# Kernel tuning notes

Hardware: AMD Instinct MI355X
Metric: run time of the kernel (lower is better)

## Reference

```python
import jax, jax.numpy as jnp
import numpy as np

N_NODES = 50000
N_EDGES = 25000
NNZ = 800000
IN_DIM = 256
OUT_DIM = 256


def setup_inputs() -> dict:
    key = jax.random.key(0)
    k1, k2, k3, k4, k5 = jax.random.split(key, 5)
    X = jax.random.normal(k1, (N_NODES, IN_DIM), dtype=jnp.float32)
    node_idx = jax.random.randint(k2, (NNZ,), 0, N_NODES, dtype=jnp.int64)
    edge_idx = jax.random.randint(k3, (NNZ,), 0, N_EDGES, dtype=jnp.int64)
    # Xavier-uniform-ish weight, zero bias (matches reset_parameters)
    limit = float(np.sqrt(6.0 / (IN_DIM + OUT_DIM)))
    W = jax.random.uniform(k4, (IN_DIM, OUT_DIM), dtype=jnp.float32, minval=-limit, maxval=limit)
    b = jnp.zeros((OUT_DIM,), dtype=jnp.float32)
    return {"X": X, "node_idx": node_idx, "edge_idx": edge_idx, "W": W, "b": b}


def reference(X, node_idx, edge_idx, W, b):
    # Y = X @ W + b  -- dense GEMM
    Y = X @ W + b  # [N, out_dim]

    ones = jnp.ones(node_idx.shape[0], dtype=Y.dtype)
    # D_v = rowsum(H)^-0.5 (inf -> 0); D_e = colsum(H)^-1 (inf -> 0)
    deg_v = jax.ops.segment_sum(ones, node_idx, num_segments=N_NODES)
    deg_e = jax.ops.segment_sum(ones, edge_idx, num_segments=N_EDGES)
    d_v = jnp.where(deg_v > 0, deg_v ** -0.5, 0.0)  # [N]
    d_e = jnp.where(deg_e > 0, 1.0 / deg_e, 0.0)    # [E]

    # step1 = H^T @ (D_v X): gather scaled node rows, scatter-add into edges
    Z = d_v[:, None] * Y                                   # [N, out_dim]
    step1 = jax.ops.segment_sum(Z[node_idx], edge_idx, num_segments=N_EDGES)  # [E, out_dim]
    # step2 = D_e @ step1
    step2 = d_e[:, None] * step1                           # [E, out_dim]
    # step3 = H @ step2: gather edge rows, scatter-add into nodes
    step3 = jax.ops.segment_sum(step2[edge_idx], node_idx, num_segments=N_NODES)  # [N, out_dim]
    # final = D_v @ step3
    return d_v[:, None] * step3
```

## Files before the change

kernel.cpp:

```cpp
#include <hip/hip_runtime.h>

#define N_NODES 50000
#define N_EDGES 25000
#define NNZ     800000
#define DIM     256

#define CAP_E 88
#define CAP_V 56

#define NBE 98
#define NBV 196
#define CE_COARSE 8800
#define CV_COARSE 4500
#define NNZ_PB 2048
#define P1_BLOCKS 391

#define B_A1   0
#define B_CE   0
#define B_CV   3449600
#define B_CSRE 12800000
#define B_CSRV 17200000
#define B_WT   22800000
#define B_CURV 22931072
#define B_CURE 23131072
#define B_CCUR 23331072
#define B_DV   23332248

typedef __attribute__((ext_vector_type(8))) short s8v;
typedef __attribute__((ext_vector_type(4))) float f4v;

__device__ __forceinline__ unsigned short f2bf(float f) {
    unsigned u = __float_as_uint(f);
    u = (u + 0x7FFFu + ((u >> 16) & 1u)) >> 16;
    return (unsigned short)u;
}
__device__ __forceinline__ float bf2f(unsigned short h) {
    return __uint_as_float(((unsigned)h) << 16);
}

__global__ __launch_bounds__(256) void k_prep(
        const float* __restrict__ W,
        const int* __restrict__ node_idx, const int* __restrict__ edge_idx,
        unsigned short* __restrict__ WTb,
        unsigned* __restrict__ ccurE, unsigned* __restrict__ ccurV,
        unsigned* __restrict__ coarseE, unsigned* __restrict__ coarseV) {
    if (blockIdx.x < 32) {
        int t = blockIdx.x * 256 + threadIdx.x;
        int n = t >> 5;
        int k0 = (t & 31) * 8;
        unsigned short o[8];
#pragma unroll
        for (int j = 0; j < 8; ++j) o[j] = f2bf(W[(size_t)(k0 + j) * DIM + n]);
        *(s8v*)(WTb + (size_t)n * DIM + k0) = *(const s8v*)o;
        return;
    }

    __shared__ unsigned histE[NBE], histV[NBV], baseE[NBE], baseV[NBV];
    __shared__ unsigned offE[NBE], offV[NBV];
    __shared__ unsigned nEs, nVs;
    __shared__ unsigned bufE[NNZ_PB], dstE[NNZ_PB];
    __shared__ unsigned bufV[NNZ_PB], dstV[NNZ_PB];
    const int tid = threadIdx.x;
    const int pb  = blockIdx.x - 32;
    const int base = pb * NNZ_PB;

    if (tid < NBE) histE[tid] = 0;
    if (tid < NBV) histV[tid] = 0;
    __syncthreads();

    int idx0 = base + tid * 4;
    int idx1 = base + 1024 + tid * 4;
    bool ok0 = idx0 < NNZ, ok1 = idx1 < NNZ;
    int4 v0 = ok0 ? *(const int4*)(node_idx + idx0) : (int4){0,0,0,0};
    int4 e0 = ok0 ? *(const int4*)(edge_idx + idx0) : (int4){0,0,0,0};
    int4 v1 = ok1 ? *(const int4*)(node_idx + idx1) : (int4){0,0,0,0};
    int4 e1 = ok1 ? *(const int4*)(edge_idx + idx1) : (int4){0,0,0,0};
    int vv[8] = {v0.x, v0.y, v0.z, v0.w, v1.x, v1.y, v1.z, v1.w};
    int ee[8] = {e0.x, e0.y, e0.z, e0.w, e1.x, e1.y, e1.z, e1.w};

    unsigned short locE[8], locV[8];
#pragma unroll
    for (int j = 0; j < 8; ++j) {
        bool ok = (j < 4) ? ok0 : ok1;
        if (ok) {
            locE[j] = (unsigned short)atomicAdd(&histE[ee[j] >> 8], 1u);
            locV[j] = (unsigned short)atomicAdd(&histV[vv[j] >> 8], 1u);
        }
    }
    __syncthreads();
    if (tid < NBE) baseE[tid] = atomicAdd(&ccurE[tid], histE[tid]);
    if (tid < NBV) baseV[tid] = atomicAdd(&ccurV[tid], histV[tid]);
    if (tid == 0) { unsigned r = 0; for (int b = 0; b < NBE; ++b) { offE[b] = r; r += histE[b]; } nEs = r; }
    if (tid == 1) { unsigned r = 0; for (int b = 0; b < NBV; ++b) { offV[b] = r; r += histV[b]; } nVs = r; }
    __syncthreads();

#pragma unroll
    for (int j = 0; j < 8; ++j) {
        bool ok = (j < 4) ? ok0 : ok1;
        if (ok) {
            unsigned e = (unsigned)ee[j], v = (unsigned)vv[j];
            unsigned be = e >> 8, bv = v >> 8;
            unsigned se = offE[be] + locE[j];
            unsigned pe = baseE[be] + locE[j];
            bufE[se] = ((e & 255u) << 16) | v;
            dstE[se] = (pe < CE_COARSE) ? (be * CE_COARSE + pe) : 0xFFFFFFFFu;
            unsigned sv = offV[bv] + locV[j];
            unsigned pv = baseV[bv] + locV[j];
            bufV[sv] = ((v & 255u) << 16) | e;
            dstV[sv] = (pv < CV_COARSE) ? (bv * CV_COARSE + pv) : 0xFFFFFFFFu;
        }
    }
    __syncthreads();

    unsigned nE = nEs, nV = nVs;
    for (unsigned i = tid; i < nE; i += 256) {
        unsigned d = dstE[i];
        if (d != 0xFFFFFFFFu) coarseE[d] = bufE[i];
    }
    for (unsigned i = tid; i < nV; i += 256) {
        unsigned d = dstV[i];
        if (d != 0xFFFFFFFFu) coarseV[d] = bufV[i];
    }
}

__global__ __launch_bounds__(1024) void k_fine(
        const unsigned* __restrict__ coarseE, const unsigned* __restrict__ coarseV,
        const unsigned* __restrict__ ccurE, const unsigned* __restrict__ ccurV,
        unsigned short* __restrict__ csrE, unsigned short* __restrict__ csrV,
        unsigned* __restrict__ cur_e, unsigned* __restrict__ cur_v,
        float* __restrict__ dv) {
    __shared__ unsigned cnt[256];
    __shared__ unsigned short slots[256 * CAP_E];
    const int tid = threadIdx.x;
    if (tid < 256) cnt[tid] = 0;
    __syncthreads();

    if (blockIdx.x < NBE) {
        int b = blockIdx.x;
        unsigned n = ccurE[b]; n = n < CE_COARSE ? n : CE_COARSE;
        const unsigned* src = coarseE + (size_t)b * CE_COARSE;
        for (unsigned i = tid; i < n; i += 1024) {
            unsigned p = src[i];
            unsigned f = p >> 16, v = p & 0xFFFFu;
            unsigned pos = atomicAdd(&cnt[f], 1u);
            if (pos < CAP_E) slots[f * CAP_E + pos] = (unsigned short)v;
        }
        __syncthreads();
        if (tid < 256) {
            int e = b * 256 + tid;
            if (e < N_EDGES) cur_e[e] = cnt[tid];
        }
        int rows = N_EDGES - b * 256; rows = rows < 256 ? rows : 256;
        unsigned words = (unsigned)rows * (CAP_E / 2);
        unsigned* dst = (unsigned*)(csrE + (size_t)b * 256 * CAP_E);
        const unsigned* s = (const unsigned*)slots;
        for (unsigned i = tid; i < words; i += 1024) dst[i] = s[i];
    } else {
        int b = blockIdx.x - NBE;
        unsigned n = ccurV[b]; n = n < CV_COARSE ? n : CV_COARSE;
        const unsigned* src = coarseV + (size_t)b * CV_COARSE;
        for (unsigned i = tid; i < n; i += 1024) {
            unsigned p = src[i];
            unsigned f = p >> 16, e = p & 0xFFFFu;
            unsigned pos = atomicAdd(&cnt[f], 1u);
            if (pos < CAP_V) slots[f * CAP_V + pos] = (unsigned short)e;
        }
        __syncthreads();
        if (tid < 256) {
            int v = b * 256 + tid;
            if (v < N_NODES) {
                unsigned c = cnt[tid];
                cur_v[v] = c;
                dv[v] = c ? __frsqrt_rn((float)c) : 0.0f;
            }
        }
        int rows = N_NODES - b * 256; rows = rows < 256 ? rows : 256;
        unsigned words = (unsigned)rows * (CAP_V / 2);
        unsigned* dst = (unsigned*)(csrV + (size_t)b * 256 * CAP_V);
        const unsigned* s = (const unsigned*)slots;
        for (unsigned i = tid; i < words; i += 1024) dst[i] = s[i];
    }
}

__global__ __launch_bounds__(256) void k_gemm_y(
        const float* __restrict__ X,
        const unsigned short* __restrict__ WT,
        const float* __restrict__ bias,
        unsigned short* __restrict__ Yb) {
    __shared__ unsigned short As[64][264];
    const int tid  = threadIdx.x;
    const int wv   = tid >> 6;
    const int lane = tid & 63;
    const int quad = lane >> 4;
    const int l16  = lane & 15;
    const int r0   = blockIdx.x * 64;
    const int nb   = wv * 64;

#pragma unroll
    for (int it = 0; it < 16; ++it) {
        int i   = tid + it * 256;
        int row = i >> 6;
        int c4  = i & 63;
        int src = r0 + row;
        src = (src < N_NODES) ? src : (N_NODES - 1);
        float4 p = *(const float4*)(X + (size_t)src * DIM + c4 * 4);
        unsigned short o[4] = {f2bf(p.x), f2bf(p.y), f2bf(p.z), f2bf(p.w)};
        *(ushort4*)(&As[row][c4 * 4]) = *(const ushort4*)o;
    }
    __syncthreads();

    f4v acc[4][4];
#pragma unroll
    for (int mt = 0; mt < 4; ++mt)
#pragma unroll
        for (int nt = 0; nt < 4; ++nt) acc[mt][nt] = (f4v){0.f, 0.f, 0.f, 0.f};

    for (int k0 = 0; k0 < DIM; k0 += 32) {
        s8v a[4], b[4];
#pragma unroll
        for (int nt = 0; nt < 4; ++nt) {
            int n = nb + nt * 16 + l16;
            b[nt] = *(const s8v*)(WT + (size_t)n * DIM + k0 + quad * 8);
        }
#pragma unroll
        for (int mt = 0; mt < 4; ++mt)
            a[mt] = *(const s8v*)(&As[mt * 16 + l16][k0 + quad * 8]);
#pragma unroll
        for (int mt = 0; mt < 4; ++mt)
#pragma unroll
            for (int nt = 0; nt < 4; ++nt)
                acc[mt][nt] = __builtin_amdgcn_mfma_f32_16x16x32_bf16(
                    a[mt], b[nt], acc[mt][nt], 0, 0, 0);
    }

    float bv[4];
#pragma unroll
    for (int nt = 0; nt < 4; ++nt) bv[nt] = bias[nb + nt * 16 + l16];

#pragma unroll
    for (int mt = 0; mt < 4; ++mt) {
#pragma unroll
        for (int reg = 0; reg < 4; ++reg) {
            int row = r0 + mt * 16 + quad * 4 + reg;
            if (row < N_NODES) {
#pragma unroll
                for (int nt = 0; nt < 4; ++nt) {
                    Yb[(size_t)row * DIM + nb + nt * 16 + l16] =
                        f2bf(acc[mt][nt][reg] + bv[nt]);
                }
            }
        }
    }
}

__global__ __launch_bounds__(256) void k_gather_edges(
        const unsigned short* __restrict__ Yb,
        const unsigned short* __restrict__ csrE,
        const unsigned* __restrict__ cur_e,
        const float* __restrict__ dv,
        unsigned short* __restrict__ S2) {
    int w = (blockIdx.x * 256 + threadIdx.x) >> 6;
    int lane = threadIdx.x & 63;
    if (w >= N_EDGES) return;
    unsigned deg = cur_e[w];
    unsigned cnt = deg < CAP_E ? deg : CAP_E;
    float sc = deg ? 1.0f / (float)deg : 0.0f;
    const unsigned short* lst = csrE + (size_t)w * CAP_E;
    unsigned idp = (lane < CAP_E / 2) ? ((const unsigned*)lst)[lane] : 0u;
    const unsigned short* xb = Yb + (size_t)lane * 4;

    float ax = 0.f, ay = 0.f, az = 0.f, aw = 0.f;

#define EFETCH(J, X0, X1, X2, X3, S0, S1, S2_, S3)                         \
    {                                                                      \
        unsigned p0 = __shfl(idp, (int)((J) >> 1));                        \
        unsigned p1 = __shfl(idp, (int)((J) >> 1) + 1);                    \
        unsigned v0 = p0 & 0xFFFFu, v1 = p0 >> 16;                         \
        unsigned v2 = p1 & 0xFFFFu, v3 = p1 >> 16;                         \
        S0 = dv[v0]; S1 = dv[v1]; S2_ = dv[v2]; S3 = dv[v3];               \
        X0 = *(const ushort4*)(xb + ((size_t)v0 << 8));                    \
        X1 = *(const ushort4*)(xb + ((size_t)v1 << 8));                    \
        X2 = *(const ushort4*)(xb + ((size_t)v2 << 8));                    \
        X3 = *(const ushort4*)(xb + ((size_t)v3 << 8));                    \
    }
#define ECONS(X0, X1, X2, X3, S0, S1, S2_, S3)                             \
    {                                                                      \
        ax = fmaf(S0, bf2f(X0.x), ax); ay = fmaf(S0, bf2f(X0.y), ay);      \
        az = fmaf(S0, bf2f(X0.z), az); aw = fmaf(S0, bf2f(X0.w), aw);      \
        ax = fmaf(S1, bf2f(X1.x), ax); ay = fmaf(S1, bf2f(X1.y), ay);      \
        az = fmaf(S1, bf2f(X1.z), az); aw = fmaf(S1, bf2f(X1.w), aw);      \
        ax = fmaf(S2_, bf2f(X2.x), ax); ay = fmaf(S2_, bf2f(X2.y), ay);    \
        az = fmaf(S2_, bf2f(X2.z), az); aw = fmaf(S2_, bf2f(X2.w), aw);    \
        ax = fmaf(S3, bf2f(X3.x), ax); ay = fmaf(S3, bf2f(X3.y), ay);      \
        az = fmaf(S3, bf2f(X3.z), az); aw = fmaf(S3, bf2f(X3.w), aw);      \
    }

    unsigned quads = cnt >> 2;
    unsigned j = 0;
    if (quads) {
        ushort4 a0, a1, a2, a3, b0, b1, b2, b3;
        float r0, r1, r2, r3, t0, t1, t2, t3;
        EFETCH(0u, a0, a1, a2, a3, r0, r1, r2, r3);
        unsigned q = 1;
        for (; q + 1 < quads; q += 2) {
            EFETCH(4u * q,      b0, b1, b2, b3, t0, t1, t2, t3);
            ECONS(a0, a1, a2, a3, r0, r1, r2, r3);
            EFETCH(4u * q + 4u, a0, a1, a2, a3, r0, r1, r2, r3);
            ECONS(b0, b1, b2, b3, t0, t1, t2, t3);
        }
        if (q < quads) {
            EFETCH(4u * q, b0, b1, b2, b3, t0, t1, t2, t3);
            ECONS(a0, a1, a2, a3, r0, r1, r2, r3);
            ECONS(b0, b1, b2, b3, t0, t1, t2, t3);
        } else {
            ECONS(a0, a1, a2, a3, r0, r1, r2, r3);
        }
        j = quads << 2;
    }
    for (; j < cnt; ++j) {
        unsigned p = __shfl(idp, (int)(j >> 1));
        unsigned v = (j & 1) ? (p >> 16) : (p & 0xFFFFu);
        float s = dv[v];
        ushort4 x = *(const ushort4*)(xb + ((size_t)v << 8));
        ax = fmaf(s, bf2f(x.x), ax); ay = fmaf(s, bf2f(x.y), ay);
        az = fmaf(s, bf2f(x.z), az); aw = fmaf(s, bf2f(x.w), aw);
    }
#undef EFETCH
#undef ECONS

    ushort4 o = {f2bf(sc * ax), f2bf(sc * ay), f2bf(sc * az), f2bf(sc * aw)};
    *(ushort4*)(S2 + (size_t)w * DIM + lane * 4) = o;
}

__global__ __launch_bounds__(256) void k_gather_nodes(
        const unsigned short* __restrict__ S2,
        const unsigned short* __restrict__ csrV,
        const unsigned* __restrict__ cur_v,
        const float* __restrict__ dv,
        float* __restrict__ out) {
    int w = (blockIdx.x * 256 + threadIdx.x) >> 6;
    int lane = threadIdx.x & 63;
    if (w >= N_NODES) return;
    unsigned cnt = cur_v[w]; cnt = cnt < CAP_V ? cnt : CAP_V;
    const unsigned short* lst = csrV + (size_t)w * CAP_V;
    unsigned idp = (lane < CAP_V / 2) ? ((const unsigned*)lst)[lane] : 0u;
    const unsigned short* sb = S2 + (size_t)lane * 4;

    float ax = 0.f, ay = 0.f, az = 0.f, aw = 0.f;

#define NFETCH(J, X0, X1, X2, X3)                                          \
    {                                                                      \
        unsigned p0 = __shfl(idp, (int)((J) >> 1));                        \
        unsigned p1 = __shfl(idp, (int)((J) >> 1) + 1);                    \
        unsigned e0 = p0 & 0xFFFFu, e1 = p0 >> 16;                         \
        unsigned e2 = p1 & 0xFFFFu, e3 = p1 >> 16;                         \
        X0 = *(const ushort4*)(sb + ((size_t)e0 << 8));                    \
        X1 = *(const ushort4*)(sb + ((size_t)e1 << 8));                    \
        X2 = *(const ushort4*)(sb + ((size_t)e2 << 8));                    \
        X3 = *(const ushort4*)(sb + ((size_t)e3 << 8));                    \
    }
#define NCONS(X0, X1, X2, X3)                                              \
    {                                                                      \
        ax += (bf2f(X0.x) + bf2f(X1.x)) + (bf2f(X2.x) + bf2f(X3.x));       \
        ay += (bf2f(X0.y) + bf2f(X1.y)) + (bf2f(X2.y) + bf2f(X3.y));       \
        az += (bf2f(X0.z) + bf2f(X1.z)) + (bf2f(X2.z) + bf2f(X3.z));       \
        aw += (bf2f(X0.w) + bf2f(X1.w)) + (bf2f(X2.w) + bf2f(X3.w));       \
    }

    unsigned quads = cnt >> 2;
    unsigned j = 0;
    if (quads) {
        ushort4 a0, a1, a2, a3, b0, b1, b2, b3;
        NFETCH(0u, a0, a1, a2, a3);
        unsigned q = 1;
        for (; q + 1 < quads; q += 2) {
            NFETCH(4u * q,      b0, b1, b2, b3);
            NCONS(a0, a1, a2, a3);
            NFETCH(4u * q + 4u, a0, a1, a2, a3);
            NCONS(b0, b1, b2, b3);
        }
        if (q < quads) {
            NFETCH(4u * q, b0, b1, b2, b3);
            NCONS(a0, a1, a2, a3);
            NCONS(b0, b1, b2, b3);
        } else {
            NCONS(a0, a1, a2, a3);
        }
        j = quads << 2;
    }
    for (; j < cnt; ++j) {
        unsigned p = __shfl(idp, (int)(j >> 1));
        unsigned e = (j & 1) ? (p >> 16) : (p & 0xFFFFu);
        ushort4 x = *(const ushort4*)(sb + ((size_t)e << 8));
        ax += bf2f(x.x); ay += bf2f(x.y); az += bf2f(x.z); aw += bf2f(x.w);
    }
#undef NFETCH
#undef NCONS

    float s = dv[w];
    float4 o = {s * ax, s * ay, s * az, s * aw};
    *(float4*)(out + (size_t)w * DIM + lane * 4) = o;
}

extern "C" void kernel_launch(void* const* d_in, const int* in_sizes, int n_in,
                              void* d_out, int out_size, void* d_ws, size_t ws_size,
                              hipStream_t stream) {
    (void)in_sizes; (void)n_in; (void)out_size; (void)ws_size;
    const float* X        = (const float*)d_in[0];
    const int*   node_idx = (const int*)d_in[1];
    const int*   edge_idx = (const int*)d_in[2];
    const float* W        = (const float*)d_in[3];
    const float* bias     = (const float*)d_in[4];
    float* out = (float*)d_out;
    char*  ws  = (char*)d_ws;

    unsigned short* S2      = (unsigned short*)(ws + B_A1);
    unsigned*       coarseE = (unsigned*)(ws + B_CE);
    unsigned*       coarseV = (unsigned*)(ws + B_CV);
    unsigned short* csrE    = (unsigned short*)(ws + B_CSRE);
    unsigned short* csrV    = (unsigned short*)(ws + B_CSRV);
    unsigned short* WTb     = (unsigned short*)(ws + B_WT);
    unsigned*       cur_v   = (unsigned*)(ws + B_CURV);
    unsigned*       cur_e   = (unsigned*)(ws + B_CURE);
    unsigned*       ccurE   = (unsigned*)(ws + B_CCUR);
    unsigned*       ccurV   = ccurE + NBE;
    float*          dv      = (float*)(ws + B_DV);

    unsigned short* Yb = (unsigned short*)d_out;

    (void)hipMemsetAsync(ccurE, 0, (NBE + NBV) * sizeof(unsigned), stream);

    k_prep<<<32 + P1_BLOCKS, 256, 0, stream>>>(W, node_idx, edge_idx,
                                               WTb, ccurE, ccurV, coarseE, coarseV);
    k_fine<<<NBE + NBV, 1024, 0, stream>>>(coarseE, coarseV, ccurE, ccurV,
                                           csrE, csrV, cur_e, cur_v, dv);
    k_gemm_y<<<(N_NODES + 63) / 64, 256, 0, stream>>>(X, WTb, bias, Yb);
    k_gather_edges<<<(N_EDGES * 64 + 255) / 256, 256, 0, stream>>>(
        Yb, csrE, cur_e, dv, S2);
    k_gather_nodes<<<(N_NODES * 64 + 255) / 256, 256, 0, stream>>>(
        S2, csrV, cur_v, dv, out);
}
```

Before: 252.4 us.

## Merge GEMM and fine CSR bucketing into one launch, parallelize prefix scans

The dense X@W GEMM and the fine-grained CSR construction now run as one 1024-thread kernel. The first blocks each compute four 64-row GEMM tiles, staging K in two halves to fit shared memory, and the remaining blocks do the per-bucket fine sort. This removes one launch and lets the independent GEMM and CSR work overlap on the GPU. In the prep kernel the serial single-thread prefix sums over the bucket histograms become a parallel Hillis-Steele scan, and the CSR slot copy-out uses 16-byte stores. The trade-offs are extra barriers in the GEMM halves and larger 1024-thread GEMM blocks, which may lower occupancy.

```diff
diff --git a/kernel.cpp b/kernel.cpp
--- a/kernel.cpp
+++ b/kernel.cpp
@@ -14,6 +14,7 @@
 #define CV_COARSE 4500
 #define NNZ_PB 2048
 #define P1_BLOCKS 391
+#define GY_BLOCKS 196
 
 #define B_A1   0
 #define B_CE   0
@@ -57,6 +58,7 @@
 
     __shared__ unsigned histE[NBE], histV[NBV], baseE[NBE], baseV[NBV];
     __shared__ unsigned offE[NBE], offV[NBV];
+    __shared__ unsigned scanE[256], scanV[256];
     __shared__ unsigned nEs, nVs;
     __shared__ unsigned bufE[NNZ_PB], dstE[NNZ_PB];
     __shared__ unsigned bufV[NNZ_PB], dstV[NNZ_PB];
@@ -90,8 +92,20 @@
     __syncthreads();
     if (tid < NBE) baseE[tid] = atomicAdd(&ccurE[tid], histE[tid]);
     if (tid < NBV) baseV[tid] = atomicAdd(&ccurV[tid], histV[tid]);
-    if (tid == 0) { unsigned r = 0; for (int b = 0; b < NBE; ++b) { offE[b] = r; r += histE[b]; } nEs = r; }
-    if (tid == 1) { unsigned r = 0; for (int b = 0; b < NBV; ++b) { offV[b] = r; r += histV[b]; } nVs = r; }
+    scanE[tid] = (tid < NBE) ? histE[tid] : 0u;
+    scanV[tid] = (tid < NBV) ? histV[tid] : 0u;
+    __syncthreads();
+    for (int off = 1; off < 256; off <<= 1) {
+        unsigned tE = (tid >= off) ? scanE[tid - off] : 0u;
+        unsigned tV = (tid >= off) ? scanV[tid - off] : 0u;
+        __syncthreads();
+        scanE[tid] += tE;
+        scanV[tid] += tV;
+        __syncthreads();
+    }
+    if (tid < NBE) offE[tid] = scanE[tid] - histE[tid];
+    if (tid < NBV) offV[tid] = scanV[tid] - histV[tid];
+    if (tid == 0) { nEs = scanE[255]; nVs = scanV[255]; }
     __syncthreads();
 
 #pragma unroll
@@ -123,20 +137,100 @@
     }
 }
 
-__global__ __launch_bounds__(1024) void k_fine(
+__global__ __launch_bounds__(1024) void k_mid(
+        const float* __restrict__ X,
+        const unsigned short* __restrict__ WT,
+        const float* __restrict__ bias,
+        unsigned short* __restrict__ Yb,
         const unsigned* __restrict__ coarseE, const unsigned* __restrict__ coarseV,
         const unsigned* __restrict__ ccurE, const unsigned* __restrict__ ccurV,
         unsigned short* __restrict__ csrE, unsigned short* __restrict__ csrV,
         unsigned* __restrict__ cur_e, unsigned* __restrict__ cur_v,
         float* __restrict__ dv) {
-    __shared__ unsigned cnt[256];
-    __shared__ unsigned short slots[256 * CAP_E];
+    __shared__ __align__(16) char smem[69632];
     const int tid = threadIdx.x;
+
+    if (blockIdx.x < GY_BLOCKS) {
+        const int sub  = tid >> 8;
+        const int stid = tid & 255;
+        const int lane = stid & 63;
+        const int wv   = stid >> 6;
+        const int quad = lane >> 4;
+        const int l16  = lane & 15;
+        const int r0   = (blockIdx.x * 4 + sub) * 64;
+        const int nb   = wv * 64;
+        unsigned short (*As)[136] =
+            (unsigned short (*)[136])(smem + sub * 17408);
+
+        f4v acc[4][4];
+#pragma unroll
+        for (int mt = 0; mt < 4; ++mt)
+#pragma unroll
+            for (int nt = 0; nt < 4; ++nt) acc[mt][nt] = (f4v){0.f, 0.f, 0.f, 0.f};
+
+        for (int h = 0; h < 2; ++h) {
+            __syncthreads();
+#pragma unroll
+            for (int it = 0; it < 8; ++it) {
+                int i   = stid + it * 256;
+                int row = i >> 5;
+                int c4  = i & 31;
+                int src = r0 + row;
+                src = (src < N_NODES) ? src : (N_NODES - 1);
+                float4 p = *(const float4*)(X + (size_t)src * DIM + h * 128 + c4 * 4);
+                unsigned short o[4] = {f2bf(p.x), f2bf(p.y), f2bf(p.z), f2bf(p.w)};
+                *(ushort4*)(&As[row][c4 * 4]) = *(const ushort4*)o;
+            }
+            __syncthreads();
+
+            for (int k0l = 0; k0l < 128; k0l += 32) {
+                s8v a[4], b[4];
+#pragma unroll
+                for (int nt = 0; nt < 4; ++nt) {
+                    int n = nb + nt * 16 + l16;
+                    b[nt] = *(const s8v*)(WT + (size_t)n * DIM + h * 128 + k0l + quad * 8);
+                }
+#pragma unroll
+                for (int mt = 0; mt < 4; ++mt)
+                    a[mt] = *(const s8v*)(&As[mt * 16 + l16][k0l + quad * 8]);
+#pragma unroll
+                for (int mt = 0; mt < 4; ++mt)
+#pragma unroll
+                    for (int nt = 0; nt < 4; ++nt)
+                        acc[mt][nt] = __builtin_amdgcn_mfma_f32_16x16x32_bf16(
+                            a[mt], b[nt], acc[mt][nt], 0, 0, 0);
+            }
+        }
+
+        float bv[4];
+#pragma unroll
+        for (int nt = 0; nt < 4; ++nt) bv[nt] = bias[nb + nt * 16 + l16];
+
+#pragma unroll
+        for (int mt = 0; mt < 4; ++mt) {
+#pragma unroll
+            for (int reg = 0; reg < 4; ++reg) {
+                int row = r0 + mt * 16 + quad * 4 + reg;
+                if (row < N_NODES) {
+#pragma unroll
+                    for (int nt = 0; nt < 4; ++nt) {
+                        Yb[(size_t)row * DIM + nb + nt * 16 + l16] =
+                            f2bf(acc[mt][nt][reg] + bv[nt]);
+                    }
+                }
+            }
+        }
+        return;
+    }
+
+    unsigned*       cnt   = (unsigned*)smem;
+    unsigned short* slots = (unsigned short*)(smem + 1024);
+    const int fb = blockIdx.x - GY_BLOCKS;
     if (tid < 256) cnt[tid] = 0;
     __syncthreads();
 
-    if (blockIdx.x < NBE) {
-        int b = blockIdx.x;
+    if (fb < NBE) {
+        int b = fb;
         unsigned n = ccurE[b]; n = n < CE_COARSE ? n : CE_COARSE;
         const unsigned* src = coarseE + (size_t)b * CE_COARSE;
         for (unsigned i = tid; i < n; i += 1024) {
@@ -151,12 +245,12 @@
             if (e < N_EDGES) cur_e[e] = cnt[tid];
         }
         int rows = N_EDGES - b * 256; rows = rows < 256 ? rows : 256;
-        unsigned words = (unsigned)rows * (CAP_E / 2);
-        unsigned* dst = (unsigned*)(csrE + (size_t)b * 256 * CAP_E);
-        const unsigned* s = (const unsigned*)slots;
-        for (unsigned i = tid; i < words; i += 1024) dst[i] = s[i];
+        unsigned q4 = (unsigned)rows * (CAP_E / 2) / 4;
+        uint4* dst = (uint4*)(csrE + (size_t)b * 256 * CAP_E);
+        const uint4* s = (const uint4*)slots;
+        for (unsigned i = tid; i < q4; i += 1024) dst[i] = s[i];
     } else {
-        int b = blockIdx.x - NBE;
+        int b = fb - NBE;
         unsigned n = ccurV[b]; n = n < CV_COARSE ? n : CV_COARSE;
         const unsigned* src = coarseV + (size_t)b * CV_COARSE;
         for (unsigned i = tid; i < n; i += 1024) {
@@ -175,81 +269,10 @@
             }
         }
         int rows = N_NODES - b * 256; rows = rows < 256 ? rows : 256;
-        unsigned words = (unsigned)rows * (CAP_V / 2);
-        unsigned* dst = (unsigned*)(csrV + (size_t)b * 256 * CAP_V);
-        const unsigned* s = (const unsigned*)slots;
-        for (unsigned i = tid; i < words; i += 1024) dst[i] = s[i];
-    }
-}
-
-__global__ __launch_bounds__(256) void k_gemm_y(
-        const float* __restrict__ X,
-        const unsigned short* __restrict__ WT,
-        const float* __restrict__ bias,
-        unsigned short* __restrict__ Yb) {
-    __shared__ unsigned short As[64][264];
-    const int tid  = threadIdx.x;
-    const int wv   = tid >> 6;
-    const int lane = tid & 63;
-    const int quad = lane >> 4;
-    const int l16  = lane & 15;
-    const int r0   = blockIdx.x * 64;
-    const int nb   = wv * 64;
-
-#pragma unroll
-    for (int it = 0; it < 16; ++it) {
-        int i   = tid + it * 256;
-        int row = i >> 6;
-        int c4  = i & 63;
-        int src = r0 + row;
-        src = (src < N_NODES) ? src : (N_NODES - 1);
-        float4 p = *(const float4*)(X + (size_t)src * DIM + c4 * 4);
-        unsigned short o[4] = {f2bf(p.x), f2bf(p.y), f2bf(p.z), f2bf(p.w)};
-        *(ushort4*)(&As[row][c4 * 4]) = *(const ushort4*)o;
-    }
-    __syncthreads();
-
-    f4v acc[4][4];
-#pragma unroll
-    for (int mt = 0; mt < 4; ++mt)
-#pragma unroll
-        for (int nt = 0; nt < 4; ++nt) acc[mt][nt] = (f4v){0.f, 0.f, 0.f, 0.f};
-
-    for (int k0 = 0; k0 < DIM; k0 += 32) {
-        s8v a[4], b[4];
-#pragma unroll
-        for (int nt = 0; nt < 4; ++nt) {
-            int n = nb + nt * 16 + l16;
-            b[nt] = *(const s8v*)(WT + (size_t)n * DIM + k0 + quad * 8);
-        }
-#pragma unroll
-        for (int mt = 0; mt < 4; ++mt)
-            a[mt] = *(const s8v*)(&As[mt * 16 + l16][k0 + quad * 8]);
-#pragma unroll
-        for (int mt = 0; mt < 4; ++mt)
-#pragma unroll
-            for (int nt = 0; nt < 4; ++nt)
-                acc[mt][nt] = __builtin_amdgcn_mfma_f32_16x16x32_bf16(
-                    a[mt], b[nt], acc[mt][nt], 0, 0, 0);
-    }
-
-    float bv[4];
-#pragma unroll
-    for (int nt = 0; nt < 4; ++nt) bv[nt] = bias[nb + nt * 16 + l16];
-
-#pragma unroll
-    for (int mt = 0; mt < 4; ++mt) {
-#pragma unroll
-        for (int reg = 0; reg < 4; ++reg) {
-            int row = r0 + mt * 16 + quad * 4 + reg;
-            if (row < N_NODES) {
-#pragma unroll
-                for (int nt = 0; nt < 4; ++nt) {
-                    Yb[(size_t)row * DIM + nb + nt * 16 + l16] =
-                        f2bf(acc[mt][nt][reg] + bv[nt]);
-                }
-            }
-        }
+        unsigned q4 = (unsigned)rows * (CAP_V / 2) / 4;
+        uint4* dst = (uint4*)(csrV + (size_t)b * 256 * CAP_V);
+        const uint4* s = (const uint4*)slots;
+        for (unsigned i = tid; i < q4; i += 1024) dst[i] = s[i];
     }
 }
 
@@ -432,9 +455,9 @@
 
     k_prep<<<32 + P1_BLOCKS, 256, 0, stream>>>(W, node_idx, edge_idx,
                                                WTb, ccurE, ccurV, coarseE, coarseV);
-    k_fine<<<NBE + NBV, 1024, 0, stream>>>(coarseE, coarseV, ccurE, ccurV,
-                                           csrE, csrV, cur_e, cur_v, dv);
-    k_gemm_y<<<(N_NODES + 63) / 64, 256, 0, stream>>>(X, WTb, bias, Yb);
+    k_mid<<<GY_BLOCKS + NBE + NBV, 1024, 0, stream>>>(
+        X, WTb, bias, Yb, coarseE, coarseV, ccurE, ccurV,
+        csrE, csrV, cur_e, cur_v, dv);
     k_gather_edges<<<(N_EDGES * 64 + 255) / 256, 256, 0, stream>>>(
         Yb, csrE, cur_e, dv, S2);
     k_gather_nodes<<<(N_NODES * 64 + 255) / 256, 256, 0, stream>>>(
```

Result: faster. 245.5 us (-2.7%).
